# Optimization experiments

Measured on AMD Instinct MI355X. Metric: run time of the kernel, lower is better.

Reference implementation:

```python
import jax, jax.numpy as jnp
import numpy as np


def setup_inputs() -> dict:
    key = jax.random.key(0)
    k1, k2, k3, k4 = jax.random.split(key, 4)
    B, D_e, D_o, T, H, W = 4, 128, 512, 8, 32, 32
    return {
        "memory_in": jax.random.normal(k1, (B, D_e, T, H, W), dtype=jnp.float32),
        "memory_out": jax.random.normal(k2, (B, D_o, T, H, W), dtype=jnp.float32),
        "query_in": jax.random.normal(k3, (B, D_e, H, W), dtype=jnp.float32),
        "query_out": jax.random.normal(k4, (B, D_o, H, W), dtype=jnp.float32),
    }


def reference(memory_in, memory_out, query_in, query_out):
    B, D_e, T, H, W = memory_in.shape
    D_o = memory_out.shape[1]
    N = T * H * W   # memory keys
    M = H * W       # query positions
    mi = memory_in.reshape(B, D_e, N)      # [B, D_e, N]
    qi = query_in.reshape(B, D_e, M)       # [B, D_e, M]
    # scores: [B, N, M], scaled dot-product, softmax over memory axis (N)
    scale = 1.0 / np.sqrt(D_e).astype(np.float32)
    prob = jnp.einsum('bdn,bdm->bnm', mi, qi) * scale
    prob = jax.nn.softmax(prob, axis=1)
    mo = memory_out.reshape(B, D_o, N)      # [B, D_o, N]
    memory = jnp.einsum('bdn,bnm->bdm', mo, prob).reshape(B, D_o, H, W)
    out = jnp.concatenate([memory, query_out], axis=1)  # [B, 2*D_o, H, W]
    return out, prob
```

## Files before the change

### kernel.cpp

```cpp
#include <hip/hip_runtime.h>
#include <math.h>
#include <stdint.h>

constexpr int B_  = 4;
constexpr int DE_ = 128;
constexpr int DO_ = 512;
constexpr int N_  = 8192;
constexpr int M_  = 1024;
constexpr int NCHUNK_ = 32;
constexpr int SPLITK_ = 4;
constexpr int KCHUNK_ = N_ / SPLITK_;

typedef __attribute__((ext_vector_type(8))) short bf16x8;
typedef __attribute__((ext_vector_type(8))) unsigned short u16x8;
typedef __attribute__((ext_vector_type(4))) float f32x4;

static __device__ __forceinline__ uint16_t f2bf(float f) {
    uint32_t u = __builtin_bit_cast(uint32_t, f);
    u += 0x7fffu + ((u >> 16) & 1u);
    return (uint16_t)(u >> 16);
}

__global__ __launch_bounds__(256) void k_scores(const float* __restrict__ mi,
                                                const float* __restrict__ qi,
                                                float* __restrict__ S) {
    __shared__ float As[32][64];
    __shared__ float Bs[32][64];
    const int m0 = blockIdx.x * 64;
    const int n0 = blockIdx.y * 64;
    const int b  = blockIdx.z;
    const int tid = threadIdx.x;
    const int tx = tid & 15;
    const int ty = tid >> 4;

    const float* miB = mi + (size_t)b * DE_ * N_;
    const float* qiB = qi + (size_t)b * DE_ * M_;

    float acc[4][4] = {};

    for (int k0 = 0; k0 < DE_; k0 += 32) {
        #pragma unroll
        for (int t = 0; t < 8; ++t) {
            int e = tid + t * 256;
            int kk = e >> 6, nn = e & 63;
            As[kk][nn] = miB[(size_t)(k0 + kk) * N_ + n0 + nn];
            Bs[kk][nn] = qiB[(size_t)(k0 + kk) * M_ + m0 + nn];
        }
        __syncthreads();
        #pragma unroll
        for (int kk = 0; kk < 32; ++kk) {
            float a[4], p[4];
            #pragma unroll
            for (int i = 0; i < 4; ++i) a[i] = As[kk][ty * 4 + i];
            #pragma unroll
            for (int j = 0; j < 4; ++j) p[j] = Bs[kk][tx * 4 + j];
            #pragma unroll
            for (int i = 0; i < 4; ++i)
                #pragma unroll
                for (int j = 0; j < 4; ++j)
                    acc[i][j] = fmaf(a[i], p[j], acc[i][j]);
        }
        __syncthreads();
    }

    const float scale = 0.08838834764831845f;
    float* Sp = S + (size_t)b * N_ * M_;
    #pragma unroll
    for (int i = 0; i < 4; ++i) {
        float4 v = make_float4(acc[i][0] * scale, acc[i][1] * scale,
                               acc[i][2] * scale, acc[i][3] * scale);
        *(float4*)&Sp[(size_t)(n0 + ty * 4 + i) * M_ + m0 + tx * 4] = v;
    }
}

__global__ __launch_bounds__(256) void k_colstats(const float* __restrict__ S,
                                                  float* __restrict__ pmax,
                                                  float* __restrict__ psum) {
    const int m = blockIdx.x * 256 + threadIdx.x;
    const int c = blockIdx.y;
    const int b = blockIdx.z;
    const float* Sp = S + (size_t)b * N_ * M_ + (size_t)c * 256 * M_ + m;
    float mx = -INFINITY, sm = 0.f;
    for (int n = 0; n < 256; ++n) {
        float x = Sp[(size_t)n * M_];
        float mnew = fmaxf(mx, x);
        sm = sm * __expf(mx - mnew) + __expf(x - mnew);
        mx = mnew;
    }
    size_t idx = ((size_t)b * NCHUNK_ + c) * M_ + m;
    pmax[idx] = mx;
    psum[idx] = sm;
}

__global__ __launch_bounds__(256) void k_reduce(const float* __restrict__ pmax,
                                                const float* __restrict__ psum,
                                                float* __restrict__ gmax,
                                                float* __restrict__ ginv) {
    const int g = blockIdx.x * 256 + threadIdx.x;
    const int b = g >> 10;
    const int m = g & (M_ - 1);
    float pm[NCHUNK_];
    float mx = -INFINITY;
    #pragma unroll
    for (int c = 0; c < NCHUNK_; ++c) {
        pm[c] = pmax[((size_t)b * NCHUNK_ + c) * M_ + m];
        mx = fmaxf(mx, pm[c]);
    }
    float sm = 0.f;
    #pragma unroll
    for (int c = 0; c < NCHUNK_; ++c) {
        sm += psum[((size_t)b * NCHUNK_ + c) * M_ + m] * __expf(pm[c] - mx);
    }
    gmax[g] = mx;
    ginv[g] = 1.0f / sm;
}

__global__ __launch_bounds__(256) void k_normalize_t(float* __restrict__ S,
                                                     const float* __restrict__ gmax,
                                                     const float* __restrict__ ginv,
                                                     uint16_t* __restrict__ Pt) {
    __shared__ float T[64][65];
    const int m0 = blockIdx.x * 64;
    const int n0 = blockIdx.y * 64;
    const int b  = blockIdx.z;
    const int t  = threadIdx.x;
    const int c  = t & 15;
    const int rr = t >> 4;

    float4 gm = *(const float4*)&gmax[b * M_ + m0 + c * 4];
    float4 gi = *(const float4*)&ginv[b * M_ + m0 + c * 4];
    float* Sp = S + (size_t)b * N_ * M_;

    #pragma unroll
    for (int it = 0; it < 4; ++it) {
        int r = rr + it * 16;
        size_t idx = (size_t)(n0 + r) * M_ + m0 + c * 4;
        float4 v = *(float4*)&Sp[idx];
        v.x = __expf(v.x - gm.x) * gi.x;
        v.y = __expf(v.y - gm.y) * gi.y;
        v.z = __expf(v.z - gm.z) * gi.z;
        v.w = __expf(v.w - gm.w) * gi.w;
        *(float4*)&Sp[idx] = v;
        T[r][c * 4 + 0] = v.x;
        T[r][c * 4 + 1] = v.y;
        T[r][c * 4 + 2] = v.z;
        T[r][c * 4 + 3] = v.w;
    }
    __syncthreads();

    const int ml = t >> 2;
    const int ns = t & 3;
    uint16_t* PtB = Pt + ((size_t)b * M_ + m0 + ml) * N_ + n0 + ns * 16;
    u16x8 s0, s1;
    #pragma unroll
    for (int jj = 0; jj < 8; ++jj) s0[jj] = f2bf(T[ns * 16 + jj][ml]);
    #pragma unroll
    for (int jj = 0; jj < 8; ++jj) s1[jj] = f2bf(T[ns * 16 + 8 + jj][ml]);
    *(u16x8*)&PtB[0] = s0;
    *(u16x8*)&PtB[8] = s1;
}

__global__ __launch_bounds__(256) void k_moconv(const float* __restrict__ mo,
                                                uint16_t* __restrict__ mo16) {
    const size_t base = ((size_t)blockIdx.x * 256 + threadIdx.x) * 16;
    float4 v0 = *(const float4*)&mo[base + 0];
    float4 v1 = *(const float4*)&mo[base + 4];
    float4 v2 = *(const float4*)&mo[base + 8];
    float4 v3 = *(const float4*)&mo[base + 12];
    u16x8 o0, o1;
    o0[0] = f2bf(v0.x); o0[1] = f2bf(v0.y); o0[2] = f2bf(v0.z); o0[3] = f2bf(v0.w);
    o0[4] = f2bf(v1.x); o0[5] = f2bf(v1.y); o0[6] = f2bf(v1.z); o0[7] = f2bf(v1.w);
    o1[0] = f2bf(v2.x); o1[1] = f2bf(v2.y); o1[2] = f2bf(v2.z); o1[3] = f2bf(v2.w);
    o1[4] = f2bf(v3.x); o1[5] = f2bf(v3.y); o1[6] = f2bf(v3.z); o1[7] = f2bf(v3.w);
    *(u16x8*)&mo16[base + 0] = o0;
    *(u16x8*)&mo16[base + 8] = o1;
}

__global__ __launch_bounds__(256) void k_pv_mfma(const uint16_t* __restrict__ mo16,
                                                 const uint16_t* __restrict__ Pt,
                                                 float* __restrict__ part) {
    __shared__ uint16_t Asm[128 * 88];
    __shared__ uint16_t Psm[128 * 88];
    const int m0 = blockIdx.x * 128;
    const int d0 = blockIdx.y * 128;
    const int b  = blockIdx.z >> 2;
    const int sk = blockIdx.z & 3;
    const int tid = threadIdx.x;

    const uint16_t* moB = mo16 + (size_t)b * DO_ * N_;
    const uint16_t* PtB = Pt   + (size_t)b * M_  * N_;

    const int srow = tid >> 3;
    const int sseg = tid & 7;

    const int w  = tid >> 6;
    const int wd = w >> 1, wm = w & 1;
    const int l  = tid & 63;
    const int lr = l & 15;
    const int lg = l >> 4;

    f32x4 acc[4][4] = {};

    for (int n0 = sk * KCHUNK_; n0 < (sk + 1) * KCHUNK_; n0 += 64) {
        #pragma unroll
        for (int i = 0; i < 4; ++i) {
            int r = srow + i * 32;
            *(bf16x8*)&Asm[r * 88 + sseg * 8] =
                *(const bf16x8*)&moB[(size_t)(d0 + r) * N_ + n0 + sseg * 8];
            *(bf16x8*)&Psm[r * 88 + sseg * 8] =
                *(const bf16x8*)&PtB[(size_t)(m0 + r) * N_ + n0 + sseg * 8];
        }
        __syncthreads();
        #pragma unroll
        for (int kk = 0; kk < 64; kk += 32) {
            bf16x8 a[4], p[4];
            #pragma unroll
            for (int i = 0; i < 4; ++i)
                a[i] = *(const bf16x8*)&Asm[(wd * 64 + i * 16 + lr) * 88 + kk + lg * 8];
            #pragma unroll
            for (int j = 0; j < 4; ++j)
                p[j] = *(const bf16x8*)&Psm[(wm * 64 + j * 16 + lr) * 88 + kk + lg * 8];
            #pragma unroll
            for (int i = 0; i < 4; ++i)
                #pragma unroll
                for (int j = 0; j < 4; ++j)
                    acc[i][j] = __builtin_amdgcn_mfma_f32_16x16x32_bf16(
                        a[i], p[j], acc[i][j], 0, 0, 0);
        }
        __syncthreads();
    }

    float* pp = part + ((size_t)(sk * B_ + b) * DO_ + d0) * M_;
    #pragma unroll
    for (int i = 0; i < 4; ++i)
        #pragma unroll
        for (int j = 0; j < 4; ++j)
            #pragma unroll
            for (int r = 0; r < 4; ++r) {
                int d = wd * 64 + i * 16 + lg * 4 + r;
                int m = wm * 64 + j * 16 + lr;
                pp[(size_t)d * M_ + m0 + m] = acc[i][j][r];
            }
}

__global__ __launch_bounds__(256) void k_pvreduce(const float* __restrict__ part,
                                                  float* __restrict__ out) {
    constexpr size_t OUTSZ = (size_t)B_ * DO_ * M_;
    const size_t i = (size_t)blockIdx.x * 256 + threadIdx.x;
    const size_t e = i * 4;
    float4 a = *(const float4*)&part[e];
    float4 b = *(const float4*)&part[OUTSZ + e];
    float4 c = *(const float4*)&part[2 * OUTSZ + e];
    float4 d = *(const float4*)&part[3 * OUTSZ + e];
    a.x += b.x + c.x + d.x;
    a.y += b.y + c.y + d.y;
    a.z += b.z + c.z + d.z;
    a.w += b.w + c.w + d.w;
    const int bb = (int)(e / ((size_t)DO_ * M_));
    const size_t rem = e % ((size_t)DO_ * M_);
    *(float4*)&out[(size_t)bb * 2 * DO_ * M_ + rem] = a;
}

__global__ __launch_bounds__(256) void k_normalize(float* __restrict__ S,
                                                   const float* __restrict__ gmax,
                                                   const float* __restrict__ ginv) {
    const size_t total4 = (size_t)B_ * N_ * M_ / 4;
    for (size_t i = (size_t)blockIdx.x * 256 + threadIdx.x; i < total4;
         i += (size_t)gridDim.x * 256) {
        size_t e = i * 4;
        int b = (int)(e / ((size_t)N_ * M_));
        int m = (int)(e & (M_ - 1));
        float4 v = ((float4*)S)[i];
        float4 gm = *(const float4*)&gmax[b * M_ + m];
        float4 gi = *(const float4*)&ginv[b * M_ + m];
        v.x = __expf(v.x - gm.x) * gi.x;
        v.y = __expf(v.y - gm.y) * gi.y;
        v.z = __expf(v.z - gm.z) * gi.z;
        v.w = __expf(v.w - gm.w) * gi.w;
        ((float4*)S)[i] = v;
    }
}

__global__ __launch_bounds__(256) void k_pv(const float* __restrict__ mo,
                                            const float* __restrict__ P,
                                            float* __restrict__ out) {
    __shared__ float As[32][68];
    __shared__ float Ps[32][64];
    const int m0 = blockIdx.x * 64;
    const int d0 = blockIdx.y * 64;
    const int b  = blockIdx.z;
    const int tid = threadIdx.x;
    const int tx = tid & 15;
    const int ty = tid >> 4;

    const float* moB = mo + (size_t)b * DO_ * N_;
    const float* PB  = P  + (size_t)b * N_ * M_;

    float acc[4][4] = {};

    for (int n0 = 0; n0 < N_; n0 += 32) {
        #pragma unroll
        for (int t = 0; t < 8; ++t) {
            int e = tid + t * 256;
            int dd = e >> 5, nn = e & 31;
            As[nn][dd] = moB[(size_t)(d0 + dd) * N_ + n0 + nn];
        }
        #pragma unroll
        for (int t = 0; t < 8; ++t) {
            int e = tid + t * 256;
            int kk = e >> 6, mm = e & 63;
            Ps[kk][mm] = PB[(size_t)(n0 + kk) * M_ + m0 + mm];
        }
        __syncthreads();
        #pragma unroll
        for (int kk = 0; kk < 32; ++kk) {
            float a[4], p[4];
            #pragma unroll
            for (int i = 0; i < 4; ++i) a[i] = As[kk][ty * 4 + i];
            #pragma unroll
            for (int j = 0; j < 4; ++j) p[j] = Ps[kk][tx * 4 + j];
            #pragma unroll
            for (int i = 0; i < 4; ++i)
                #pragma unroll
                for (int j = 0; j < 4; ++j)
                    acc[i][j] = fmaf(a[i], p[j], acc[i][j]);
        }
        __syncthreads();
    }

    float* outB = out + (size_t)b * 2 * DO_ * M_;
    #pragma unroll
    for (int i = 0; i < 4; ++i) {
        float4 v = make_float4(acc[i][0], acc[i][1], acc[i][2], acc[i][3]);
        *(float4*)&outB[(size_t)(d0 + ty * 4 + i) * M_ + m0 + tx * 4] = v;
    }
}

__global__ __launch_bounds__(256) void k_copyq(const float* __restrict__ q,
                                               float* __restrict__ out) {
    const size_t i = (size_t)blockIdx.x * 256 + threadIdx.x;
    const size_t e = i * 4;
    const int b = (int)(e / ((size_t)DO_ * M_));
    const size_t r = e % ((size_t)DO_ * M_);
    float4 v = *(const float4*)&q[e];
    *(float4*)&out[(size_t)b * 2 * DO_ * M_ + (size_t)DO_ * M_ + r] = v;
}

extern "C" void kernel_launch(void* const* d_in, const int* in_sizes, int n_in,
                              void* d_out, int out_size, void* d_ws, size_t ws_size,
                              hipStream_t stream) {
    const float* mi = (const float*)d_in[0];
    const float* mo = (const float*)d_in[1];
    const float* qi = (const float*)d_in[2];
    const float* qo = (const float*)d_in[3];

    float* out  = (float*)d_out;
    float* prob = out + (size_t)B_ * 2 * DO_ * M_;

    float* pmax = (float*)d_ws;
    float* psum = pmax + (size_t)B_ * NCHUNK_ * M_;
    float* gmax = psum + (size_t)B_ * NCHUNK_ * M_;
    float* ginv = gmax + (size_t)B_ * M_;
    uint16_t* Pt   = (uint16_t*)(ginv + B_ * M_);
    uint16_t* mo16 = Pt + (size_t)B_ * M_ * N_;
    float*    part = (float*)(mo16 + (size_t)B_ * DO_ * N_);
    const size_t need =
        (size_t)((char*)(part + (size_t)SPLITK_ * B_ * DO_ * M_) - (char*)d_ws);

    k_scores  <<<dim3(M_ / 64, N_ / 64, B_), 256, 0, stream>>>(mi, qi, prob);
    k_colstats<<<dim3(M_ / 256, NCHUNK_, B_), 256, 0, stream>>>(prob, pmax, psum);
    k_reduce  <<<dim3(B_ * M_ / 256), 256, 0, stream>>>(pmax, psum, gmax, ginv);

    if (ws_size >= need) {
        k_moconv     <<<dim3((B_ * DO_ * N_ / 16) / 256), 256, 0, stream>>>(mo, mo16);
        k_normalize_t<<<dim3(M_ / 64, N_ / 64, B_), 256, 0, stream>>>(prob, gmax, ginv, Pt);
        k_pv_mfma    <<<dim3(M_ / 128, DO_ / 128, B_ * SPLITK_), 256, 0, stream>>>(mo16, Pt, part);
        k_pvreduce   <<<dim3((B_ * DO_ * M_ / 4) / 256), 256, 0, stream>>>(part, out);
    } else {
        k_normalize<<<dim3(2048), 256, 0, stream>>>(prob, gmax, ginv);
        k_pv       <<<dim3(M_ / 64, DO_ / 64, B_), 256, 0, stream>>>(mo, prob, out);
    }
    k_copyq<<<dim3((B_ * DO_ * M_ / 4) / 256), 256, 0, stream>>>(qo, out);
}
```

Baseline: 467.7 us.

## Compute attention scores with bf16 MFMA after transposing inputs to bf16

Adds a kernel that transposes and converts memory_in and query_in to bf16 in a K-contiguous layout. A new 128x128-tile score kernel then uses 16x16x32 bf16 MFMA instructions in place of the scalar fp32 FMA GEMM. It targets the compute cost of the scores GEMM but adds two conversion passes and lowers score precision to bf16 inputs. The fp32 path is kept as a fallback when the workspace is too small.

```diff
diff --git a/kernel.cpp b/kernel.cpp
--- a/kernel.cpp
+++ b/kernel.cpp
@@ -19,6 +19,91 @@
     uint32_t u = __builtin_bit_cast(uint32_t, f);
     u += 0x7fffu + ((u >> 16) & 1u);
     return (uint16_t)(u >> 16);
+}
+
+__global__ __launch_bounds__(256) void k_tconv(const float* __restrict__ src,
+                                               uint16_t* __restrict__ dst,
+                                               int ncols) {
+    const int n    = blockIdx.x * 64 + (threadIdx.x & 63);
+    const int dseg = threadIdx.x >> 6;
+    const int b    = blockIdx.y;
+    const float* s = src + (size_t)b * DE_ * ncols + n;
+    uint16_t*    d = dst + ((size_t)b * ncols + n) * DE_;
+    #pragma unroll
+    for (int db = 0; db < 4; ++db) {
+        int d0 = db * 32 + dseg * 8;
+        u16x8 o;
+        #pragma unroll
+        for (int q = 0; q < 8; ++q) o[q] = f2bf(s[(size_t)(d0 + q) * ncols]);
+        *(u16x8*)&d[d0] = o;
+    }
+}
+
+__global__ __launch_bounds__(256) void k_scores_mfma(const uint16_t* __restrict__ mit,
+                                                     const uint16_t* __restrict__ qit,
+                                                     float* __restrict__ S) {
+    __shared__ uint16_t Asm[128 * 88];
+    __shared__ uint16_t Bsm[128 * 88];
+    const int m0 = blockIdx.x * 128;
+    const int n0 = blockIdx.y * 128;
+    const int b  = blockIdx.z;
+    const int tid = threadIdx.x;
+
+    const uint16_t* A  = mit + (size_t)b * N_ * DE_;
+    const uint16_t* Bq = qit + (size_t)b * M_ * DE_;
+
+    const int srow = tid >> 3;
+    const int sseg = tid & 7;
+
+    const int w  = tid >> 6;
+    const int wn = w >> 1, wm = w & 1;
+    const int l  = tid & 63;
+    const int lr = l & 15;
+    const int lg = l >> 4;
+
+    f32x4 acc[4][4] = {};
+
+    for (int k0 = 0; k0 < DE_; k0 += 64) {
+        #pragma unroll
+        for (int i = 0; i < 4; ++i) {
+            int r = srow + i * 32;
+            *(bf16x8*)&Asm[r * 88 + sseg * 8] =
+                *(const bf16x8*)&A[(size_t)(n0 + r) * DE_ + k0 + sseg * 8];
+            *(bf16x8*)&Bsm[r * 88 + sseg * 8] =
+                *(const bf16x8*)&Bq[(size_t)(m0 + r) * DE_ + k0 + sseg * 8];
+        }
+        __syncthreads();
+        #pragma unroll
+        for (int kk = 0; kk < 64; kk += 32) {
+            bf16x8 a[4], p[4];
+            #pragma unroll
+            for (int i = 0; i < 4; ++i)
+                a[i] = *(const bf16x8*)&Asm[(wn * 64 + i * 16 + lr) * 88 + kk + lg * 8];
+            #pragma unroll
+            for (int j = 0; j < 4; ++j)
+                p[j] = *(const bf16x8*)&Bsm[(wm * 64 + j * 16 + lr) * 88 + kk + lg * 8];
+            #pragma unroll
+            for (int i = 0; i < 4; ++i)
+                #pragma unroll
+                for (int j = 0; j < 4; ++j)
+                    acc[i][j] = __builtin_amdgcn_mfma_f32_16x16x32_bf16(
+                        a[i], p[j], acc[i][j], 0, 0, 0);
+        }
+        __syncthreads();
+    }
+
+    const float scale = 0.08838834764831845f;
+    float* Sp = S + (size_t)b * N_ * M_;
+    #pragma unroll
+    for (int i = 0; i < 4; ++i)
+        #pragma unroll
+        for (int j = 0; j < 4; ++j)
+            #pragma unroll
+            for (int r = 0; r < 4; ++r) {
+                int n = n0 + wn * 64 + i * 16 + lg * 4 + r;
+                int m = m0 + wm * 64 + j * 16 + lr;
+                Sp[(size_t)n * M_ + m] = acc[i][j][r] * scale;
+            }
 }
 
 __global__ __launch_bounds__(256) void k_scores(const float* __restrict__ mi,
@@ -364,14 +449,25 @@
     uint16_t* Pt   = (uint16_t*)(ginv + B_ * M_);
     uint16_t* mo16 = Pt + (size_t)B_ * M_ * N_;
     float*    part = (float*)(mo16 + (size_t)B_ * DO_ * N_);
-    const size_t need =
-        (size_t)((char*)(part + (size_t)SPLITK_ * B_ * DO_ * M_) - (char*)d_ws);
-
-    k_scores  <<<dim3(M_ / 64, N_ / 64, B_), 256, 0, stream>>>(mi, qi, prob);
+    uint16_t* mit  = (uint16_t*)(part + (size_t)SPLITK_ * B_ * DO_ * M_);
+    uint16_t* qit  = mit + (size_t)B_ * N_ * DE_;
+    const size_t need_fast =
+        (size_t)((char*)mit - (char*)d_ws);
+    const size_t need_full =
+        (size_t)((char*)(qit + (size_t)B_ * M_ * DE_) - (char*)d_ws);
+
+    if (ws_size >= need_full) {
+        k_tconv      <<<dim3(N_ / 64, B_), 256, 0, stream>>>(mi, mit, N_);
+        k_tconv      <<<dim3(M_ / 64, B_), 256, 0, stream>>>(qi, qit, M_);
+        k_scores_mfma<<<dim3(M_ / 128, N_ / 128, B_), 256, 0, stream>>>(mit, qit, prob);
+    } else {
+        k_scores<<<dim3(M_ / 64, N_ / 64, B_), 256, 0, stream>>>(mi, qi, prob);
+    }
+
     k_colstats<<<dim3(M_ / 256, NCHUNK_, B_), 256, 0, stream>>>(prob, pmax, psum);
     k_reduce  <<<dim3(B_ * M_ / 256), 256, 0, stream>>>(pmax, psum, gmax, ginv);
 
-    if (ws_size >= need) {
+    if (ws_size >= need_fast) {
         k_moconv     <<<dim3((B_ * DO_ * N_ / 16) / 256), 256, 0, stream>>>(mo, mo16);
         k_normalize_t<<<dim3(M_ / 64, N_ / 64, B_), 256, 0, stream>>>(prob, gmax, ginv, Pt);
         k_pv_mfma    <<<dim3(M_ / 128, DO_ / 128, B_ * SPLITK_), 256, 0, stream>>>(mo16, Pt, part);
```

Result: faster. 388.6 us (-16.9%).
